# Kernel tuning notes

Hardware: AMD Instinct MI355X
Metric: run time of the kernel (lower is better)

Reference implementation:

```python
import jax, jax.numpy as jnp
import numpy as np

NUM_HEADS = 12


def setup_inputs() -> dict:
    key = jax.random.key(0)
    ks = jax.random.split(key, 7)
    n_node, n_graph, E = 1024, 4, 768
    return {
        "query": jax.random.normal(ks[0], (n_node, n_graph, E), jnp.float32),
        "attn_bias": jax.random.normal(ks[1], (n_graph * NUM_HEADS, n_node, n_node), jnp.float32),
        "node_non_padding_mask": jax.random.randint(ks[2], (n_graph, n_node), 0, 2).astype(bool),
        "W_in": jax.random.normal(ks[3], (3 * E, E), jnp.float32) * (E ** -0.5),
        "b_in": jax.random.normal(ks[4], (3 * E,), jnp.float32) * 0.02,
        "W_out": jax.random.normal(ks[5], (E, E), jnp.float32) * (E ** -0.5),
        "b_out": jax.random.normal(ks[6], (E,), jnp.float32) * 0.02,
    }


def reference(query, attn_bias, node_non_padding_mask, W_in, b_in, W_out, b_out):
    n_node, n_graph, E = query.shape
    H = NUM_HEADS
    hd = E // H
    scaling = hd ** -0.5

    # fused qkv projection, then chunk along last dim (torch .chunk(3, -1))
    qkv = query @ W_in.T + b_in                      # [N, B, 3E]
    q, k, v = jnp.split(qkv, 3, axis=-1)             # each [N, B, E]

    def to_bh(x):
        # [N, B, E] -> [N, B*H, hd] -> [B*H, N, hd]
        return x.reshape(n_node, n_graph * H, hd).transpose(1, 0, 2)

    q = to_bh(q) * scaling
    k = to_bh(k)
    v = to_bh(v)

    attn_weights = jnp.einsum('bnd,bmd->bnm', q, k) + attn_bias   # [B*H, N, N]
    attn_probs = jax.nn.softmax(attn_weights, axis=-1)            # dropout=0 (eval)
    attn = jnp.einsum('bnm,bmd->bnd', attn_probs, v)              # [B*H, N, hd]
    attn = attn.transpose(1, 0, 2).reshape(n_node, n_graph, E)

    out = attn @ W_out.T + b_out                                   # [N, B, E]
    mask = node_non_padding_mask.T[:, :, None]                     # [N, B, 1]
    return jnp.where(mask, out, 0.0)
```

## Files before the change

### kernel.cpp

```cpp
#include <hip/hip_runtime.h>
#include <hip/hip_bf16.h>

#define NNODE 1024
#define NGRAPH 4
#define EDIM 768
#define NH 12
#define HD 64
#define NBH 48
#define MTOK 4096
#define QKVN 2304

typedef __attribute__((ext_vector_type(8))) short bf16x8;
typedef __attribute__((ext_vector_type(4))) short bf16x4;
typedef __attribute__((ext_vector_type(4))) float f32x4;

static __device__ __forceinline__ float s2f(short x) {
    union { unsigned u; float f; } c;
    c.u = ((unsigned)(unsigned short)x) << 16;
    return c.f;
}
static __device__ __forceinline__ short f2s(float f) {
    union { float f; unsigned u; } c; c.f = f;
    unsigned r = (c.u + 0x7FFFu + ((c.u >> 16) & 1u)) >> 16;
    return (short)r;
}

__global__ __launch_bounds__(256) void gemm_bt(
    const float* __restrict__ A,
    const float* __restrict__ B,
    const float* __restrict__ bias,
    void* __restrict__ Cv,
    int M, int N, int K, int mode, const int* __restrict__ mask)
{
    const int BK = 32, LDK = 40;
    __shared__ __align__(16) short As[64 * LDK];
    __shared__ __align__(16) short Bs[64 * LDK];

    const int m0 = blockIdx.x * 64;
    const int n0 = blockIdx.y * 64;
    const int t = threadIdx.x;
    const int w = t >> 6, l = t & 63;
    const int wm = (w & 1) * 32, wn = (w >> 1) * 32;
    const int ldr = t >> 2;
    const int ldc = (t & 3) * 8;

    f32x4 acc[2][2];
    #pragma unroll
    for (int i = 0; i < 2; i++)
        #pragma unroll
        for (int j = 0; j < 2; j++)
            acc[i][j] = (f32x4){0.f, 0.f, 0.f, 0.f};

    const int lr = l & 15;
    const int lk = (l >> 4) * 8;

    for (int kt = 0; kt < K; kt += BK) {
        const float* ap = A + (size_t)(m0 + ldr) * K + kt + ldc;
        const float* bp = B + (size_t)(n0 + ldr) * K + kt + ldc;
        float4 a0 = *(const float4*)(ap);
        float4 a1 = *(const float4*)(ap + 4);
        float4 b0 = *(const float4*)(bp);
        float4 b1 = *(const float4*)(bp + 4);
        bf16x8 av, bv;
        av[0] = f2s(a0.x); av[1] = f2s(a0.y); av[2] = f2s(a0.z); av[3] = f2s(a0.w);
        av[4] = f2s(a1.x); av[5] = f2s(a1.y); av[6] = f2s(a1.z); av[7] = f2s(a1.w);
        bv[0] = f2s(b0.x); bv[1] = f2s(b0.y); bv[2] = f2s(b0.z); bv[3] = f2s(b0.w);
        bv[4] = f2s(b1.x); bv[5] = f2s(b1.y); bv[6] = f2s(b1.z); bv[7] = f2s(b1.w);
        *(bf16x8*)(&As[ldr * LDK + ldc]) = av;
        *(bf16x8*)(&Bs[ldr * LDK + ldc]) = bv;
        __syncthreads();

        bf16x8 af0 = *(const bf16x8*)(&As[(wm + lr) * LDK + lk]);
        bf16x8 af1 = *(const bf16x8*)(&As[(wm + 16 + lr) * LDK + lk]);
        bf16x8 bf0 = *(const bf16x8*)(&Bs[(wn + lr) * LDK + lk]);
        bf16x8 bf1 = *(const bf16x8*)(&Bs[(wn + 16 + lr) * LDK + lk]);

        acc[0][0] = __builtin_amdgcn_mfma_f32_16x16x32_bf16(af0, bf0, acc[0][0], 0, 0, 0);
        acc[0][1] = __builtin_amdgcn_mfma_f32_16x16x32_bf16(af0, bf1, acc[0][1], 0, 0, 0);
        acc[1][0] = __builtin_amdgcn_mfma_f32_16x16x32_bf16(af1, bf0, acc[1][0], 0, 0, 0);
        acc[1][1] = __builtin_amdgcn_mfma_f32_16x16x32_bf16(af1, bf1, acc[1][1], 0, 0, 0);
        __syncthreads();
    }

    const int lq = l >> 4;
    short* Cb = (short*)Cv;
    float* Cf = (float*)Cv;
    #pragma unroll
    for (int i = 0; i < 2; i++) {
        #pragma unroll
        for (int j = 0; j < 2; j++) {
            const int col = n0 + wn + j * 16 + lr;
            const float bcol = bias[col];
            #pragma unroll
            for (int r = 0; r < 4; r++) {
                const int row = m0 + wm + i * 16 + lq * 4 + r;
                float v = acc[i][j][r] + bcol;
                if (mode == 0) {
                    if (col < EDIM) v *= 0.125f;
                    Cb[(size_t)row * N + col] = f2s(v);
                } else {
                    const int nn = row >> 2, bb = row & 3;
                    if (mask[bb * NNODE + nn] == 0) v = 0.f;
                    Cf[(size_t)row * N + col] = v;
                }
            }
        }
    }
}

#define FLDK 72
#define FLDP 72
__global__ __launch_bounds__(256) void flash_attn(
    const short* __restrict__ qkv,
    const float* __restrict__ attn_bias,
    float* __restrict__ attn)
{
    __shared__ __align__(16) short Ks[64 * FLDK];
    __shared__ __align__(16) short Vt[64 * FLDK];
    __shared__ __align__(16) short Ps[4][16 * FLDP];

    const int bh = blockIdx.y;
    const int b = bh / NH, h = bh - b * NH;
    const int q0 = blockIdx.x * 64;
    const int t = threadIdx.x;
    const int w = t >> 6, l = t & 63;
    const int c = l & 15, g = l >> 4;

    const int qrow = q0 + w * 16 + c;
    const short* qptr = qkv + (size_t)(qrow * NGRAPH + b) * QKVN + h * HD + g * 8;
    bf16x8 qa0 = *(const bf16x8*)(qptr);
    bf16x8 qa1 = *(const bf16x8*)(qptr + 32);

    const int skrow = t >> 3;
    const int scol8 = (t & 7) * 8;
    const int sxor = scol8 & 0x38;

    float m_st[4], l_st[4];
    f32x4 o[4];
    #pragma unroll
    for (int r = 0; r < 4; r++) { m_st[r] = -3e38f; l_st[r] = 0.f; }
    #pragma unroll
    for (int ct = 0; ct < 4; ct++) o[ct] = (f32x4){0.f, 0.f, 0.f, 0.f};

    const float* brow_base = attn_bias + (size_t)bh * NNODE * NNODE;

    for (int k0 = 0; k0 < NNODE; k0 += 64) {
        __syncthreads();
        #pragma unroll
        for (int p = 0; p < 2; p++) {
            const int kr = skrow + p * 32;
            const short* kvp = qkv + (size_t)((k0 + kr) * NGRAPH + b) * QKVN + h * HD + scol8;
            bf16x8 kk = *(const bf16x8*)(kvp + EDIM);
            bf16x8 vv = *(const bf16x8*)(kvp + 2 * EDIM);
            *(bf16x8*)&Ks[kr * FLDK + scol8] = kk;
            const int kks = kr ^ sxor;
            #pragma unroll
            for (int j = 0; j < 8; j++)
                Vt[(scol8 + j) * FLDK + kks] = vv[j];
        }
        __syncthreads();

        f32x4 s[4];
        #pragma unroll
        for (int ct = 0; ct < 4; ct++) {
            #pragma unroll
            for (int r = 0; r < 4; r++)
                s[ct][r] = brow_base[(size_t)(q0 + w * 16 + g * 4 + r) * NNODE + k0 + ct * 16 + c];
        }
        #pragma unroll
        for (int ct = 0; ct < 4; ct++) {
            bf16x8 kb0 = *(const bf16x8*)&Ks[(ct * 16 + c) * FLDK + g * 8];
            bf16x8 kb1 = *(const bf16x8*)&Ks[(ct * 16 + c) * FLDK + 32 + g * 8];
            s[ct] = __builtin_amdgcn_mfma_f32_16x16x32_bf16(qa0, kb0, s[ct], 0, 0, 0);
            s[ct] = __builtin_amdgcn_mfma_f32_16x16x32_bf16(qa1, kb1, s[ct], 0, 0, 0);
        }

        float mn[4], alpha[4];
        #pragma unroll
        for (int r = 0; r < 4; r++) {
            float mx = fmaxf(fmaxf(s[0][r], s[1][r]), fmaxf(s[2][r], s[3][r]));
            #pragma unroll
            for (int off = 1; off < 16; off <<= 1)
                mx = fmaxf(mx, __shfl_xor(mx, off));
            mn[r] = fmaxf(m_st[r], mx);
            alpha[r] = __expf(m_st[r] - mn[r]);
            m_st[r] = mn[r];
        }
        float rs[4] = {0.f, 0.f, 0.f, 0.f};
        #pragma unroll
        for (int ct = 0; ct < 4; ct++) {
            #pragma unroll
            for (int r = 0; r < 4; r++) {
                float pv = __expf(s[ct][r] - mn[r]);
                s[ct][r] = pv;
                rs[r] += pv;
            }
        }
        #pragma unroll
        for (int r = 0; r < 4; r++) {
            #pragma unroll
            for (int off = 1; off < 16; off <<= 1)
                rs[r] += __shfl_xor(rs[r], off);
            l_st[r] = alpha[r] * l_st[r] + rs[r];
        }
        #pragma unroll
        for (int ct = 0; ct < 4; ct++)
            #pragma unroll
            for (int r = 0; r < 4; r++)
                o[ct][r] *= alpha[r];

        short* ps = &Ps[w][0];
        #pragma unroll
        for (int ct = 0; ct < 4; ct++)
            #pragma unroll
            for (int r = 0; r < 4; r++)
                ps[(g * 4 + r) * FLDP + ct * 16 + c] = f2s(s[ct][r]);

        bf16x8 pa0 = *(const bf16x8*)&ps[c * FLDP + g * 8];
        bf16x8 pa1 = *(const bf16x8*)&ps[c * FLDP + 32 + g * 8];
        #pragma unroll
        for (int ct = 0; ct < 4; ct++) {
            const int d = ct * 16 + c;
            const int x = d & 0x38;
            bf16x8 vb0 = *(const bf16x8*)&Vt[d * FLDK + ((g * 8) ^ x)];
            bf16x8 vb1 = *(const bf16x8*)&Vt[d * FLDK + ((32 + g * 8) ^ x)];
            o[ct] = __builtin_amdgcn_mfma_f32_16x16x32_bf16(pa0, vb0, o[ct], 0, 0, 0);
            o[ct] = __builtin_amdgcn_mfma_f32_16x16x32_bf16(pa1, vb1, o[ct], 0, 0, 0);
        }
    }

    float inv[4];
    #pragma unroll
    for (int r = 0; r < 4; r++) inv[r] = 1.f / l_st[r];
    #pragma unroll
    for (int ct = 0; ct < 4; ct++) {
        #pragma unroll
        for (int r = 0; r < 4; r++) {
            const int n = q0 + w * 16 + g * 4 + r;
            attn[(size_t)(n * NGRAPH + b) * EDIM + h * HD + ct * 16 + c] = o[ct][r] * inv[r];
        }
    }
}

extern "C" void kernel_launch(void* const* d_in, const int* in_sizes, int n_in,
                              void* d_out, int out_size, void* d_ws, size_t ws_size,
                              hipStream_t stream) {
    const float* query     = (const float*)d_in[0];
    const float* attn_bias = (const float*)d_in[1];
    const int*   mask      = (const int*)d_in[2];
    const float* W_in      = (const float*)d_in[3];
    const float* b_in      = (const float*)d_in[4];
    const float* W_out     = (const float*)d_in[5];
    const float* b_out     = (const float*)d_in[6];
    float* out = (float*)d_out;

    short* qkv  = (short*)d_ws;
    float* attn = (float*)(qkv + (size_t)MTOK * QKVN);

    {
        dim3 grid(MTOK / 64, QKVN / 64);
        gemm_bt<<<grid, 256, 0, stream>>>(query, W_in, b_in, qkv,
                                          MTOK, QKVN, EDIM, 0, nullptr);
    }
    {
        dim3 grid(NNODE / 64, NBH);
        flash_attn<<<grid, 256, 0, stream>>>(qkv, attn_bias, attn);
    }
    {
        dim3 grid(MTOK / 64, EDIM / 64);
        gemm_bt<<<grid, 256, 0, stream>>>(attn, W_out, b_out, out,
                                          MTOK, EDIM, EDIM, 1, mask);
    }
}
```

Measured before the change: 407.7 us.

## Pre-convert GEMM operands to bf16, widen K tile, prefetch attention bias

Adds a conversion kernel that turns query, W_in and W_out into bf16 once, so the GEMM loads bf16 directly and no longer converts redundantly inside every tile. The GEMM K-step grows from 32 to 64 with two MFMA sub-steps per stage. The attention kernel now writes its output as bf16, which halves that intermediate's traffic. It also prefetches the next bias tile into registers so the bias load overlaps with compute. The costs are three extra launches, extra workspace, and more register pressure in the attention kernel.

New measurement: 364.9 us. -10.5%, faster.

```diff
diff --git a/kernel.cpp b/kernel.cpp
--- a/kernel.cpp
+++ b/kernel.cpp
@@ -14,25 +14,32 @@
 typedef __attribute__((ext_vector_type(4))) short bf16x4;
 typedef __attribute__((ext_vector_type(4))) float f32x4;
 
-static __device__ __forceinline__ float s2f(short x) {
-    union { unsigned u; float f; } c;
-    c.u = ((unsigned)(unsigned short)x) << 16;
-    return c.f;
-}
 static __device__ __forceinline__ short f2s(float f) {
     union { float f; unsigned u; } c; c.f = f;
     unsigned r = (c.u + 0x7FFFu + ((c.u >> 16) & 1u)) >> 16;
     return (short)r;
 }
 
+__global__ __launch_bounds__(256) void cvt_bf16(
+    const float* __restrict__ in, short* __restrict__ out, int n)
+{
+    const int i = (blockIdx.x * 256 + threadIdx.x) * 8;
+    float4 a = *(const float4*)(in + i);
+    float4 b = *(const float4*)(in + i + 4);
+    bf16x8 v;
+    v[0] = f2s(a.x); v[1] = f2s(a.y); v[2] = f2s(a.z); v[3] = f2s(a.w);
+    v[4] = f2s(b.x); v[5] = f2s(b.y); v[6] = f2s(b.z); v[7] = f2s(b.w);
+    *(bf16x8*)(out + i) = v;
+}
+
 __global__ __launch_bounds__(256) void gemm_bt(
-    const float* __restrict__ A,
-    const float* __restrict__ B,
+    const short* __restrict__ A,
+    const short* __restrict__ B,
     const float* __restrict__ bias,
     void* __restrict__ Cv,
     int M, int N, int K, int mode, const int* __restrict__ mask)
 {
-    const int BK = 32, LDK = 40;
+    const int LDK = 72;
     __shared__ __align__(16) short As[64 * LDK];
     __shared__ __align__(16) short Bs[64 * LDK];
 
@@ -42,7 +49,7 @@
     const int w = t >> 6, l = t & 63;
     const int wm = (w & 1) * 32, wn = (w >> 1) * 32;
     const int ldr = t >> 2;
-    const int ldc = (t & 3) * 8;
+    const int ldc = (t & 3) * 16;
 
     f32x4 acc[2][2];
     #pragma unroll
@@ -54,31 +61,30 @@
     const int lr = l & 15;
     const int lk = (l >> 4) * 8;
 
-    for (int kt = 0; kt < K; kt += BK) {
-        const float* ap = A + (size_t)(m0 + ldr) * K + kt + ldc;
-        const float* bp = B + (size_t)(n0 + ldr) * K + kt + ldc;
-        float4 a0 = *(const float4*)(ap);
-        float4 a1 = *(const float4*)(ap + 4);
-        float4 b0 = *(const float4*)(bp);
-        float4 b1 = *(const float4*)(bp + 4);
-        bf16x8 av, bv;
-        av[0] = f2s(a0.x); av[1] = f2s(a0.y); av[2] = f2s(a0.z); av[3] = f2s(a0.w);
-        av[4] = f2s(a1.x); av[5] = f2s(a1.y); av[6] = f2s(a1.z); av[7] = f2s(a1.w);
-        bv[0] = f2s(b0.x); bv[1] = f2s(b0.y); bv[2] = f2s(b0.z); bv[3] = f2s(b0.w);
-        bv[4] = f2s(b1.x); bv[5] = f2s(b1.y); bv[6] = f2s(b1.z); bv[7] = f2s(b1.w);
-        *(bf16x8*)(&As[ldr * LDK + ldc]) = av;
-        *(bf16x8*)(&Bs[ldr * LDK + ldc]) = bv;
+    for (int kt = 0; kt < K; kt += 64) {
+        const short* ap = A + (size_t)(m0 + ldr) * K + kt + ldc;
+        const short* bp = B + (size_t)(n0 + ldr) * K + kt + ldc;
+        uint4 a0 = *(const uint4*)(ap);
+        uint4 a1 = *(const uint4*)(ap + 8);
+        uint4 b0 = *(const uint4*)(bp);
+        uint4 b1 = *(const uint4*)(bp + 8);
+        *(uint4*)(&As[ldr * LDK + ldc]) = a0;
+        *(uint4*)(&As[ldr * LDK + ldc + 8]) = a1;
+        *(uint4*)(&Bs[ldr * LDK + ldc]) = b0;
+        *(uint4*)(&Bs[ldr * LDK + ldc + 8]) = b1;
         __syncthreads();
 
-        bf16x8 af0 = *(const bf16x8*)(&As[(wm + lr) * LDK + lk]);
-        bf16x8 af1 = *(const bf16x8*)(&As[(wm + 16 + lr) * LDK + lk]);
-        bf16x8 bf0 = *(const bf16x8*)(&Bs[(wn + lr) * LDK + lk]);
-        bf16x8 bf1 = *(const bf16x8*)(&Bs[(wn + 16 + lr) * LDK + lk]);
-
-        acc[0][0] = __builtin_amdgcn_mfma_f32_16x16x32_bf16(af0, bf0, acc[0][0], 0, 0, 0);
-        acc[0][1] = __builtin_amdgcn_mfma_f32_16x16x32_bf16(af0, bf1, acc[0][1], 0, 0, 0);
-        acc[1][0] = __builtin_amdgcn_mfma_f32_16x16x32_bf16(af1, bf0, acc[1][0], 0, 0, 0);
-        acc[1][1] = __builtin_amdgcn_mfma_f32_16x16x32_bf16(af1, bf1, acc[1][1], 0, 0, 0);
+        #pragma unroll
+        for (int ks = 0; ks < 2; ks++) {
+            bf16x8 af0 = *(const bf16x8*)(&As[(wm + lr) * LDK + ks * 32 + lk]);
+            bf16x8 af1 = *(const bf16x8*)(&As[(wm + 16 + lr) * LDK + ks * 32 + lk]);
+            bf16x8 bf0 = *(const bf16x8*)(&Bs[(wn + lr) * LDK + ks * 32 + lk]);
+            bf16x8 bf1 = *(const bf16x8*)(&Bs[(wn + 16 + lr) * LDK + ks * 32 + lk]);
+            acc[0][0] = __builtin_amdgcn_mfma_f32_16x16x32_bf16(af0, bf0, acc[0][0], 0, 0, 0);
+            acc[0][1] = __builtin_amdgcn_mfma_f32_16x16x32_bf16(af0, bf1, acc[0][1], 0, 0, 0);
+            acc[1][0] = __builtin_amdgcn_mfma_f32_16x16x32_bf16(af1, bf0, acc[1][0], 0, 0, 0);
+            acc[1][1] = __builtin_amdgcn_mfma_f32_16x16x32_bf16(af1, bf1, acc[1][1], 0, 0, 0);
+        }
         __syncthreads();
     }
 
@@ -113,7 +119,7 @@
 __global__ __launch_bounds__(256) void flash_attn(
     const short* __restrict__ qkv,
     const float* __restrict__ attn_bias,
-    float* __restrict__ attn)
+    short* __restrict__ attn)
 {
     __shared__ __align__(16) short Ks[64 * FLDK];
     __shared__ __align__(16) short Vt[64 * FLDK];
@@ -142,7 +148,14 @@
     #pragma unroll
     for (int ct = 0; ct < 4; ct++) o[ct] = (f32x4){0.f, 0.f, 0.f, 0.f};
 
-    const float* brow_base = attn_bias + (size_t)bh * NNODE * NNODE;
+    const float* bp_base = attn_bias + (size_t)bh * NNODE * NNODE
+                         + (size_t)(q0 + w * 16) * NNODE;
+    float bpre[16];
+    #pragma unroll
+    for (int ct = 0; ct < 4; ct++)
+        #pragma unroll
+        for (int r = 0; r < 4; r++)
+            bpre[ct * 4 + r] = bp_base[(size_t)(g * 4 + r) * NNODE + ct * 16 + c];
 
     for (int k0 = 0; k0 < NNODE; k0 += 64) {
         __syncthreads();
@@ -162,11 +175,18 @@
 
         f32x4 s[4];
         #pragma unroll
-        for (int ct = 0; ct < 4; ct++) {
+        for (int ct = 0; ct < 4; ct++)
             #pragma unroll
             for (int r = 0; r < 4; r++)
-                s[ct][r] = brow_base[(size_t)(q0 + w * 16 + g * 4 + r) * NNODE + k0 + ct * 16 + c];
-        }
+                s[ct][r] = bpre[ct * 4 + r];
+
+        const int knext = (k0 + 64) & (NNODE - 1);
+        #pragma unroll
+        for (int ct = 0; ct < 4; ct++)
+            #pragma unroll
+            for (int r = 0; r < 4; r++)
+                bpre[ct * 4 + r] = bp_base[(size_t)(g * 4 + r) * NNODE + knext + ct * 16 + c];
+
         #pragma unroll
         for (int ct = 0; ct < 4; ct++) {
             bf16x8 kb0 = *(const bf16x8*)&Ks[(ct * 16 + c) * FLDK + g * 8];
@@ -237,7 +257,8 @@
         #pragma unroll
         for (int r = 0; r < 4; r++) {
             const int n = q0 + w * 16 + g * 4 + r;
-            attn[(size_t)(n * NGRAPH + b) * EDIM + h * HD + ct * 16 + c] = o[ct][r] * inv[r];
+            attn[(size_t)(n * NGRAPH + b) * EDIM + h * HD + ct * 16 + c] =
+                f2s(o[ct][r] * inv[r]);
         }
     }
 }
@@ -254,12 +275,19 @@
     const float* b_out     = (const float*)d_in[6];
     float* out = (float*)d_out;
 
-    short* qkv  = (short*)d_ws;
-    float* attn = (float*)(qkv + (size_t)MTOK * QKVN);
+    short* qkv     = (short*)d_ws;
+    short* attn    = qkv + (size_t)MTOK * QKVN;
+    short* q_bf    = attn + (size_t)MTOK * EDIM;
+    short* win_bf  = q_bf + (size_t)MTOK * EDIM;
+    short* wout_bf = win_bf + (size_t)QKVN * EDIM;
+
+    cvt_bf16<<<(MTOK * EDIM) / 2048, 256, 0, stream>>>(query, q_bf, MTOK * EDIM);
+    cvt_bf16<<<(QKVN * EDIM) / 2048, 256, 0, stream>>>(W_in, win_bf, QKVN * EDIM);
+    cvt_bf16<<<(EDIM * EDIM) / 2048, 256, 0, stream>>>(W_out, wout_bf, EDIM * EDIM);
 
     {
         dim3 grid(MTOK / 64, QKVN / 64);
-        gemm_bt<<<grid, 256, 0, stream>>>(query, W_in, b_in, qkv,
+        gemm_bt<<<grid, 256, 0, stream>>>(q_bf, win_bf, b_in, qkv,
                                           MTOK, QKVN, EDIM, 0, nullptr);
     }
     {
@@ -268,7 +296,7 @@
     }
     {
         dim3 grid(MTOK / 64, EDIM / 64);
-        gemm_bt<<<grid, 256, 0, stream>>>(attn, W_out, b_out, out,
+        gemm_bt<<<grid, 256, 0, stream>>>(attn, wout_bf, b_out, out,
                                           MTOK, EDIM, EDIM, 1, mask);
     }
 }
```
